# Kernel optimization log

Measured on AMD Instinct MI355X. Metric: run time of the kernel, lower is better.

Reference implementation:

```python
import jax, jax.numpy as jnp
import numpy as np

B_, L_, D_ = 4, 4096, 256
EXPAND = 2
DI_ = EXPAND * D_      # 512 inner channels
H_ = 8                 # heads
P_ = DI_ // H_         # 64 head dim
N_ = 16                # d_state
K_ = 3                 # depthwise conv kernel


def setup_inputs() -> dict:
    key = jax.random.key(0)
    ks = jax.random.split(key, 32)

    def n(i, shape, s=0.02):
        return jax.random.normal(ks[i], shape, jnp.float32) * s

    inp = {"inputs": jax.random.normal(ks[0], (B_, L_, D_), jnp.float32)}
    i = 1
    for pre in ("f_", "b_"):
        inp[pre + "in_proj_w"] = n(i, (2 * DI_, D_)); i += 1
        inp[pre + "in_proj_b"] = jnp.zeros((2 * DI_,), jnp.float32)
        inp[pre + "x_proj_w"] = n(i, (DI_ + 2 * H_ * N_, DI_)); i += 1
        inp[pre + "x_proj_b"] = jnp.zeros((DI_ + 2 * H_ * N_,), jnp.float32)
        inp[pre + "dt_bias"] = jnp.full((DI_,), -4.0, jnp.float32)  # softplus -> small dt
        inp[pre + "A_log"] = jnp.log(jnp.tile(jnp.arange(1, N_ + 1, dtype=jnp.float32), (DI_, 1)))
        inp[pre + "D_skip"] = jnp.ones((DI_,), jnp.float32)
        inp[pre + "out_proj_w"] = n(i, (D_, DI_)); i += 1
        inp[pre + "out_proj_b"] = jnp.zeros((D_,), jnp.float32)
    inp["norm_w"] = jnp.ones((D_,), jnp.float32)
    inp["norm_b"] = jnp.zeros((D_,), jnp.float32)
    inp["conv_w"] = n(20, (D_, 1, K_), 0.1)   # depthwise: (out_ch, in_ch/groups=1, k)
    inp["conv_b"] = jnp.zeros((D_,), jnp.float32)
    return inp


def _layernorm(x, w, b):
    m = x.mean(-1, keepdims=True)
    v = ((x - m) ** 2).mean(-1, keepdims=True)
    return (x - m) * jax.lax.rsqrt(v + 1e-5) * w + b


def _mh_ssm(x, in_w, in_b, xp_w, xp_b, dt_b, A_log, D_skip, out_w, out_b):
    # Multihead selective-scan SSM (Mamba-style). x: (B, L, D)
    Bsz, L, _ = x.shape
    xz = x @ in_w.T + in_b                      # (B, L, 2*DI)
    xi, z = jnp.split(xz, 2, axis=-1)
    xi = jax.nn.silu(xi)                        # (B, L, DI)
    proj = xi @ xp_w.T + xp_b                   # (B, L, DI + 2*H*N)
    dt = jax.nn.softplus(proj[..., :DI_] + dt_b)        # (B, L, DI)
    Bm = proj[..., DI_:DI_ + H_ * N_].reshape(Bsz, L, H_, N_)
    Cm = proj[..., DI_ + H_ * N_:].reshape(Bsz, L, H_, N_)
    A = -jnp.exp(A_log).reshape(H_, P_, N_)     # (H, P, N), negative
    x4 = xi.reshape(Bsz, L, H_, P_)
    dt4 = dt.reshape(Bsz, L, H_, P_)

    def step(h, t):
        xt, dtt, Bt, Ct = t                     # (B,H,P), (B,H,P), (B,H,N), (B,H,N)
        dA = jnp.exp(dtt[..., None] * A)        # (B,H,P,N)
        h = h * dA + dtt[..., None] * Bt[:, :, None, :] * xt[..., None]
        y = jnp.einsum('bhpn,bhn->bhp', h, Ct)
        return h, y

    xs = (x4.transpose(1, 0, 2, 3), dt4.transpose(1, 0, 2, 3),
          Bm.transpose(1, 0, 2, 3), Cm.transpose(1, 0, 2, 3))
    h0 = jnp.zeros((Bsz, H_, P_, N_), x.dtype)
    _, ys = jax.lax.scan(step, h0, xs)          # ys: (L,B,H,P)
    y = ys.transpose(1, 0, 2, 3).reshape(Bsz, L, DI_) + xi * D_skip
    y = y * jax.nn.silu(z)                      # gating
    return y @ out_w.T + out_b                  # (B, L, D)


def reference(inputs,
              f_in_proj_w, f_in_proj_b, f_x_proj_w, f_x_proj_b, f_dt_bias,
              f_A_log, f_D_skip, f_out_proj_w, f_out_proj_b,
              b_in_proj_w, b_in_proj_b, b_x_proj_w, b_x_proj_b, b_dt_bias,
              b_A_log, b_D_skip, b_out_proj_w, b_out_proj_b,
              norm_w, norm_b, conv_w, conv_b):
    # Cascaded bidirectional SSM: backward(flip(norm(forward(x)))) then flip back
    y1 = _mh_ssm(inputs, f_in_proj_w, f_in_proj_b, f_x_proj_w, f_x_proj_b,
                 f_dt_bias, f_A_log, f_D_skip, f_out_proj_w, f_out_proj_b)
    y1n = jnp.flip(_layernorm(y1, norm_w, norm_b), axis=1)
    y2 = _mh_ssm(y1n, b_in_proj_w, b_in_proj_b, b_x_proj_w, b_x_proj_b,
                 b_dt_bias, b_A_log, b_D_skip, b_out_proj_w, b_out_proj_b)
    out = jnp.flip(y2, axis=1)
    # locality branch: depthwise Conv1d (groups=C) + exact GELU
    xt = inputs.transpose(0, 2, 1)              # (B, C, L)
    c = jax.lax.conv_general_dilated(
        xt, conv_w, window_strides=(1,), padding=[(1, 1)],
        dimension_numbers=('NCH', 'OIH', 'NCH'), feature_group_count=D_)
    c = jax.nn.gelu(c + conv_b[None, :, None], approximate=False)
    return out + c.transpose(0, 2, 1)
```

## Files before the change

### kernel.cpp

```cpp
#include <hip/hip_runtime.h>
#include <hip/hip_bf16.h>
#include <cstdint>
#include <cstddef>

#define B_  4
#define L_  4096
#define D_  256
#define DI_ 512
#define H_  8
#define P_  64
#define N_  16
#define M_  (B_ * L_)
#define PROJ_ (DI_ + 2 * H_ * N_)

#define NC_ 128
#define CL_ (L_ / NC_)
#define NSEQ_ (B_ * H_ * P_ * N_)
#define LOG2E_ 1.4426950408889634f

typedef __bf16 bf16x8 __attribute__((ext_vector_type(8)));
typedef float f32x4 __attribute__((ext_vector_type(4)));

__device__ __forceinline__ void cp16_lds(const __hip_bfloat16* g, short* lds) {
    __builtin_amdgcn_global_load_lds(
        (const __attribute__((address_space(1))) void*)g,
        (__attribute__((address_space(3))) void*)lds, 16, 0, 0);
}

#define FS0 (M_ * D_)
#define FS1 (2 * DI_ * D_)
#define FS2 (PROJ_ * DI_)
#define FS3 (D_ * DI_)
#define FC1 (FS0 + FS1)
#define FC2 (FC1 + FS2)
#define FC3 (FC2 + FS3)
#define FC4 (FC3 + FS1)
#define FC5 (FC4 + FS2)
#define FC6 (FC5 + FS3)

__launch_bounds__(256)
__global__ void f2b_all(const float* __restrict__ i0, const float* __restrict__ i1,
                        const float* __restrict__ i2, const float* __restrict__ i3,
                        const float* __restrict__ i4, const float* __restrict__ i5,
                        const float* __restrict__ i6,
                        __hip_bfloat16* o0, __hip_bfloat16* o1, __hip_bfloat16* o2,
                        __hip_bfloat16* o3, __hip_bfloat16* o4, __hip_bfloat16* o5,
                        __hip_bfloat16* o6) {
    for (int idx = blockIdx.x * 256 + threadIdx.x; idx < FC6; idx += gridDim.x * 256) {
        const float* s; __hip_bfloat16* d; int off;
        if (idx < FS0)      { s = i0; d = o0; off = idx; }
        else if (idx < FC1) { s = i1; d = o1; off = idx - FS0; }
        else if (idx < FC2) { s = i2; d = o2; off = idx - FC1; }
        else if (idx < FC3) { s = i3; d = o3; off = idx - FC2; }
        else if (idx < FC4) { s = i4; d = o4; off = idx - FC3; }
        else if (idx < FC5) { s = i5; d = o5; off = idx - FC4; }
        else                { s = i6; d = o6; off = idx - FC5; }
        d[off] = __float2bfloat16(s[off]);
    }
}

template <int EPI>
__launch_bounds__(256)
__global__ void gemm_mfma(const __hip_bfloat16* __restrict__ A,
                          const __hip_bfloat16* __restrict__ W,
                          const float* __restrict__ bias, int Kv,
                          __hip_bfloat16* __restrict__ zb,
                          __hip_bfloat16* __restrict__ obf,
                          const float* __restrict__ aux) {
    __shared__ short As[128 * 64];
    __shared__ short Bs[128 * 64];
    const int tid = threadIdx.x;
    const int lane = tid & 63;
    const int wave = tid >> 6;
    const int bm = blockIdx.x * 128;
    const int bn = blockIdx.y * 128;
    const int wm = (wave >> 1) * 64;
    const int wn = (wave & 1) * 64;

    f32x4 acc[4][4];
#pragma unroll
    for (int i = 0; i < 4; ++i)
#pragma unroll
        for (int j = 0; j < 4; ++j) acc[i][j] = (f32x4)0.f;

    const int srow = lane >> 3;
    const int ssegx = ((lane & 7) ^ srow) * 8;
    const __hip_bfloat16* gA0 = A + (size_t)(bm + wave * 32 + srow) * Kv + ssegx;
    const __hip_bfloat16* gB0 = W + (size_t)(bn + wave * 32 + srow) * Kv + ssegx;
    short* lA0 = As + (wave * 32) * 64;
    short* lB0 = Bs + (wave * 32) * 64;

    const int fr = lane & 15;
    const int kq = lane >> 4;

    for (int k0 = 0; k0 < Kv; k0 += 64) {
#pragma unroll
        for (int rb = 0; rb < 4; ++rb) {
            cp16_lds(gA0 + (size_t)(rb * 8) * Kv + k0, lA0 + rb * 8 * 64);
            cp16_lds(gB0 + (size_t)(rb * 8) * Kv + k0, lB0 + rb * 8 * 64);
        }
        __syncthreads();
#pragma unroll
        for (int ks = 0; ks < 2; ++ks) {
            const int kgg = ks * 4 + kq;
            const int kslot = (kgg ^ (fr & 7)) * 8;
            bf16x8 af[4], bv[4];
#pragma unroll
            for (int i = 0; i < 4; ++i)
                af[i] = *reinterpret_cast<const bf16x8*>(
                    &As[(wm + i * 16 + fr) * 64 + kslot]);
#pragma unroll
            for (int j = 0; j < 4; ++j)
                bv[j] = *reinterpret_cast<const bf16x8*>(
                    &Bs[(wn + j * 16 + fr) * 64 + kslot]);
#pragma unroll
            for (int i = 0; i < 4; ++i)
#pragma unroll
                for (int j = 0; j < 4; ++j)
                    acc[i][j] = __builtin_amdgcn_mfma_f32_16x16x32_bf16(
                        af[i], bv[j], acc[i][j], 0, 0, 0);
        }
        __syncthreads();
    }

    const int n16 = lane & 15;
    const int r4 = (lane >> 4) * 4;
#pragma unroll
    for (int i = 0; i < 4; ++i) {
#pragma unroll
        for (int j = 0; j < 4; ++j) {
            const int cg = bn + wn + j * 16 + n16;
            const float bb = bias[cg];
#pragma unroll
            for (int v = 0; v < 4; ++v) {
                const int r = bm + wm + i * 16 + r4 + v;
                float val = acc[i][j][v] + bb;
                if (EPI == 1) {
                    if (cg < DI_) {
                        val = val / (1.f + __expf(-val));
                        obf[(size_t)r * DI_ + cg] = __float2bfloat16(val);
                    } else {
                        zb[(size_t)r * DI_ + cg - DI_] = __float2bfloat16(val);
                    }
                } else {
                    if (cg < DI_) {
                        const float x = val + aux[cg];
                        val = (x > 20.f) ? x : __logf(1.f + __expf(x));
                    }
                    obf[(size_t)r * PROJ_ + cg] = __float2bfloat16(val);
                }
            }
        }
    }
}

__launch_bounds__(256)
__global__ void gemm64_convout(const __hip_bfloat16* __restrict__ A,
                               const __hip_bfloat16* __restrict__ W,
                               const float* __restrict__ bias, int Kv,
                               float* __restrict__ out0,
                               const float* __restrict__ cw,
                               const float* __restrict__ cb,
                               const float* __restrict__ cinp) {
    __shared__ short As[64 * 64];
    __shared__ short Bs[64 * 64];
    const int tid = threadIdx.x;
    const int lane = tid & 63;
    const int wave = tid >> 6;
    const int bm = blockIdx.x * 64;
    const int bn = blockIdx.y * 64;
    const int wm = (wave >> 1) * 32;
    const int wn = (wave & 1) * 32;

    f32x4 acc[2][2];
#pragma unroll
    for (int i = 0; i < 2; ++i)
#pragma unroll
        for (int j = 0; j < 2; ++j) acc[i][j] = (f32x4)0.f;

    const int srow = lane >> 3;
    const int ssegx = ((lane & 7) ^ srow) * 8;
    const __hip_bfloat16* gA0 = A + (size_t)(bm + wave * 16 + srow) * Kv + ssegx;
    const __hip_bfloat16* gB0 = W + (size_t)(bn + wave * 16 + srow) * Kv + ssegx;
    short* lA0 = As + (wave * 16) * 64;
    short* lB0 = Bs + (wave * 16) * 64;

    const int fr = lane & 15;
    const int kq = lane >> 4;

    for (int k0 = 0; k0 < Kv; k0 += 64) {
#pragma unroll
        for (int rb = 0; rb < 2; ++rb) {
            cp16_lds(gA0 + (size_t)(rb * 8) * Kv + k0, lA0 + rb * 8 * 64);
            cp16_lds(gB0 + (size_t)(rb * 8) * Kv + k0, lB0 + rb * 8 * 64);
        }
        __syncthreads();
#pragma unroll
        for (int ks = 0; ks < 2; ++ks) {
            const int kgg = ks * 4 + kq;
            const int kslot = (kgg ^ (fr & 7)) * 8;
            bf16x8 af[2], bv[2];
#pragma unroll
            for (int i = 0; i < 2; ++i)
                af[i] = *reinterpret_cast<const bf16x8*>(
                    &As[(wm + i * 16 + fr) * 64 + kslot]);
#pragma unroll
            for (int j = 0; j < 2; ++j)
                bv[j] = *reinterpret_cast<const bf16x8*>(
                    &Bs[(wn + j * 16 + fr) * 64 + kslot]);
#pragma unroll
            for (int i = 0; i < 2; ++i)
#pragma unroll
                for (int j = 0; j < 2; ++j)
                    acc[i][j] = __builtin_amdgcn_mfma_f32_16x16x32_bf16(
                        af[i], bv[j], acc[i][j], 0, 0, 0);
        }
        __syncthreads();
    }

    const int n16 = lane & 15;
    const int r4 = (lane >> 4) * 4;
#pragma unroll
    for (int i = 0; i < 2; ++i) {
#pragma unroll
        for (int j = 0; j < 2; ++j) {
            const int cg = bn + wn + j * 16 + n16;
            const float bb = bias[cg];
#pragma unroll
            for (int v = 0; v < 4; ++v) {
                const int r = bm + wm + i * 16 + r4 + v;
                float val = acc[i][j][v] + bb;
                const int b = r >> 12;
                const int l = r & (L_ - 1);
                const int lo = L_ - 1 - l;
                const size_t base = ((size_t)(b << 12) + lo) * 256 + cg;
                float cv = fmaf(cinp[base], cw[cg * 3 + 1], cb[cg]);
                if (lo > 0) cv = fmaf(cinp[base - 256], cw[cg * 3 + 0], cv);
                if (lo + 1 < L_) cv = fmaf(cinp[base + 256], cw[cg * 3 + 2], cv);
                const float g = 0.5f * cv * (1.f + erff(cv * 0.70710678118654752f));
                out0[base] = val + g;
            }
        }
    }
}

__launch_bounds__(256)
__global__ void gemm_out_ln(const __hip_bfloat16* __restrict__ A,
                            const __hip_bfloat16* __restrict__ W,
                            const float* __restrict__ bias,
                            const float* __restrict__ lnw,
                            const float* __restrict__ lnb,
                            __hip_bfloat16* __restrict__ outb) {
    __shared__ short As[16 * 64];
    __shared__ short Ws[256 * 64];
    __shared__ float rs[2][4][16];
    const int tid = threadIdx.x;
    const int lane = tid & 63;
    const int wave = tid >> 6;
    const int bm = blockIdx.x * 16;
    const int Kv = DI_;

    f32x4 acc[4];
#pragma unroll
    for (int j = 0; j < 4; ++j) acc[j] = (f32x4)0.f;

    const int srow = lane >> 3;
    const int ssegx = ((lane & 7) ^ srow) * 8;
    const __hip_bfloat16* gA0 = A + (size_t)(bm + wave * 8 + srow) * Kv + ssegx;
    const __hip_bfloat16* gW0 = W + (size_t)(wave * 64 + srow) * Kv + ssegx;
    short* lA0 = As + (wave * 8) * 64;
    short* lW0 = Ws + (wave * 64) * 64;

    const int fr = lane & 15;
    const int kq = lane >> 4;

    for (int k0 = 0; k0 < Kv; k0 += 64) {
        if (wave < 2) cp16_lds(gA0 + k0, lA0);
#pragma unroll
        for (int rb = 0; rb < 8; ++rb)
            cp16_lds(gW0 + (size_t)(rb * 8) * Kv + k0, lW0 + rb * 8 * 64);
        __syncthreads();
#pragma unroll
        for (int ks = 0; ks < 2; ++ks) {
            const int kgg = ks * 4 + kq;
            const int kslot = (kgg ^ (fr & 7)) * 8;
            const bf16x8 af = *reinterpret_cast<const bf16x8*>(
                &As[fr * 64 + kslot]);
#pragma unroll
            for (int j = 0; j < 4; ++j) {
                const bf16x8 bv = *reinterpret_cast<const bf16x8*>(
                    &Ws[(wave * 64 + j * 16 + fr) * 64 + kslot]);
                acc[j] = __builtin_amdgcn_mfma_f32_16x16x32_bf16(
                    af, bv, acc[j], 0, 0, 0);
            }
        }
        __syncthreads();
    }

    const int n16 = lane & 15;
    const int r4 = (lane >> 4) * 4;
    float vals[4][4];
#pragma unroll
    for (int j = 0; j < 4; ++j) {
        const float bb = bias[wave * 64 + j * 16 + n16];
#pragma unroll
        for (int v = 0; v < 4; ++v) vals[j][v] = acc[j][v] + bb;
    }

#pragma unroll
    for (int v = 0; v < 4; ++v) {
        float s = 0.f, s2 = 0.f;
#pragma unroll
        for (int j = 0; j < 4; ++j) {
            const float t = vals[j][v];
            s += t; s2 = fmaf(t, t, s2);
        }
        s += __shfl_xor(s, 1); s2 += __shfl_xor(s2, 1);
        s += __shfl_xor(s, 2); s2 += __shfl_xor(s2, 2);
        s += __shfl_xor(s, 4); s2 += __shfl_xor(s2, 4);
        s += __shfl_xor(s, 8); s2 += __shfl_xor(s2, 8);
        if (n16 == 0) {
            rs[0][wave][r4 + v] = s;
            rs[1][wave][r4 + v] = s2;
        }
    }
    __syncthreads();

#pragma unroll
    for (int v = 0; v < 4; ++v) {
        const int row = r4 + v;
        const float ts = rs[0][0][row] + rs[0][1][row] + rs[0][2][row] + rs[0][3][row];
        const float ts2 = rs[1][0][row] + rs[1][1][row] + rs[1][2][row] + rs[1][3][row];
        const float mean = ts * (1.f / 256.f);
        const float var = ts2 * (1.f / 256.f) - mean * mean;
        const float inv = rsqrtf(var + 1e-5f);
        const int rg = bm + row;
        const int b = rg >> 12;
        const int l = rg & (L_ - 1);
        const size_t drow = (size_t)((b << 12) + (L_ - 1 - l)) * 256;
#pragma unroll
        for (int j = 0; j < 4; ++j) {
            const int cg = wave * 64 + j * 16 + n16;
            const float o = (vals[j][v] - mean) * inv * lnw[cg] + lnb[cg];
            outb[drow + cg] = __float2bfloat16(o);
        }
    }
}

__device__ __forceinline__ bool a_is_arith(const float* A2) {
    bool ok = true;
#pragma unroll
    for (int n = 1; n < N_; ++n)
        ok = ok && (fabsf(A2[n] - (float)(n + 1) * A2[0]) <= 1e-4f * fabsf(A2[n]));
    return ok;
}

__launch_bounds__(256)
__global__ void scan_chunk_state(const __hip_bfloat16* __restrict__ xi,
                                 const __hip_bfloat16* __restrict__ projb,
                                 const float* __restrict__ A_log,
                                 float* __restrict__ st_prod,
                                 float* __restrict__ st_hend) {
    __shared__ float bsh[4][CL_][16];
    const int bh = blockIdx.x;
    const int b = bh >> 3;
    const int h = bh & 7;
    const int lane = threadIdx.x & 63;
    const int wave = threadIdx.x >> 6;
    const int chunk = blockIdx.y * 4 + wave;
    const int t0 = chunk * CL_;
    const int c = h * P_ + lane;
    const int bOff = DI_ + h * N_;

    {
        const int stp = lane >> 1;
        const int half = (lane & 1) * 8;
        const __hip_bfloat16* src =
            projb + ((size_t)b * L_ + t0 + stp) * PROJ_ + bOff + half;
        const bf16x8 v = *reinterpret_cast<const bf16x8*>(src);
        float4* dst = reinterpret_cast<float4*>(&bsh[wave][stp][half]);
        dst[0] = make_float4((float)v[0], (float)v[1], (float)v[2], (float)v[3]);
        dst[1] = make_float4((float)v[4], (float)v[5], (float)v[6], (float)v[7]);
    }

    float A2[N_], hs[N_];
#pragma unroll
    for (int n = 0; n < N_; ++n) {
        A2[n] = -__expf(A_log[c * N_ + n]) * LOG2E_;
        hs[n] = 0.f;
    }
    const bool fast = a_is_arith(A2);

    const __hip_bfloat16* pDt = projb + ((size_t)b * L_ + t0) * PROJ_ + c;
    const __hip_bfloat16* px = xi + ((size_t)b * L_ + t0) * DI_ + c;
    float S = 0.f;

    if (fast) {
        float dtb[2][4], xb[2][4];
#pragma unroll
        for (int i = 0; i < 4; ++i) {
            dtb[0][i] = __bfloat162float(pDt[(size_t)i * PROJ_]);
            xb[0][i] = __bfloat162float(px[(size_t)i * DI_]);
        }
#pragma unroll
        for (int k = 0; k < CL_ / 4; ++k) {
            const int cur = k & 1, nxt = cur ^ 1;
            if (k + 1 < CL_ / 4) {
#pragma unroll
                for (int i = 0; i < 4; ++i) {
                    dtb[nxt][i] = __bfloat162float(pDt[(size_t)((k + 1) * 4 + i) * PROJ_]);
                    xb[nxt][i] = __bfloat162float(px[(size_t)((k + 1) * 4 + i) * DI_]);
                }
            }
#pragma unroll
            for (int i = 0; i < 4; ++i) {
                const int t = k * 4 + i;
                const float dt_v = dtb[cur][i];
                const float dtx = dt_v * xb[cur][i];
                const float e1 = exp2f(dt_v * A2[0]);
                S += dt_v;
                const f32x4* bp = reinterpret_cast<const f32x4*>(&bsh[wave][t][0]);
                float dA = e1;
#pragma unroll
                for (int q = 0; q < 4; ++q) {
                    const f32x4 Bq = bp[q];
#pragma unroll
                    for (int j = 0; j < 4; ++j) {
                        hs[q * 4 + j] = fmaf(hs[q * 4 + j], dA, dtx * Bq[j]);
                        dA *= e1;
                    }
                }
            }
        }
    } else {
#pragma unroll 4
        for (int t = 0; t < CL_; ++t) {
            const float dt_v = __bfloat162float(pDt[(size_t)t * PROJ_]);
            const float xv = __bfloat162float(px[(size_t)t * DI_]);
            const float dtx = dt_v * xv;
            S += dt_v;
#pragma unroll
            for (int n = 0; n < N_; ++n) {
                const float dA = exp2f(dt_v * A2[n]);
                hs[n] = fmaf(hs[n], dA, dtx * bsh[wave][t][n]);
            }
        }
    }

    const size_t s0 = (size_t)chunk * NSEQ_ + ((size_t)(bh * P_ + lane)) * N_;
#pragma unroll
    for (int n = 0; n < N_; n += 4) {
        *reinterpret_cast<float4*>(st_prod + s0 + n) =
            make_float4(exp2f(A2[n] * S), exp2f(A2[n + 1] * S),
                        exp2f(A2[n + 2] * S), exp2f(A2[n + 3] * S));
        *reinterpret_cast<float4*>(st_hend + s0 + n) =
            make_float4(hs[n], hs[n + 1], hs[n + 2], hs[n + 3]);
    }
}

__launch_bounds__(256)
__global__ void scan_combine(float* __restrict__ st_prod,
                             const float* __restrict__ st_hend) {
    const int s = blockIdx.x * 256 + threadIdx.x;
    float H = 0.f;
#pragma unroll 8
    for (int k = 0; k < NC_; ++k) {
        const size_t o = (size_t)k * NSEQ_ + s;
        const float Pv = st_prod[o];
        const float Ev = st_hend[o];
        st_prod[o] = H;
        H = fmaf(Pv, H, Ev);
    }
}

__launch_bounds__(256)
__global__ void scan_chunk_out(const __hip_bfloat16* __restrict__ xi,
                               const __hip_bfloat16* __restrict__ z,
                               const __hip_bfloat16* __restrict__ projb,
                               const float* __restrict__ A_log,
                               const float* __restrict__ D_skip,
                               const float* __restrict__ st_hin,
                               __hip_bfloat16* __restrict__ yg) {
    __shared__ float bc[4][CL_][32];
    const int bh = blockIdx.x;
    const int b = bh >> 3;
    const int h = bh & 7;
    const int lane = threadIdx.x & 63;
    const int wave = threadIdx.x >> 6;
    const int chunk = blockIdx.y * 4 + wave;
    const int t0 = chunk * CL_;
    const int c = h * P_ + lane;
    const int bOff = DI_ + h * N_;
    const int cOff = DI_ + H_ * N_ + h * N_;

    {
#pragma unroll
        for (int r = 0; r < 2; ++r) {
            const int g = r * 64 + lane;
            const int stp = g >> 2;
            const int q = g & 3;
            const int soff = (q < 2) ? (bOff + q * 8) : (cOff + (q - 2) * 8);
            const __hip_bfloat16* src =
                projb + ((size_t)b * L_ + t0 + stp) * PROJ_ + soff;
            const bf16x8 v = *reinterpret_cast<const bf16x8*>(src);
            float4* dst = reinterpret_cast<float4*>(&bc[wave][stp][q * 8]);
            dst[0] = make_float4((float)v[0], (float)v[1], (float)v[2], (float)v[3]);
            dst[1] = make_float4((float)v[4], (float)v[5], (float)v[6], (float)v[7]);
        }
    }

    float A2[N_], hs[N_];
    const size_t s0 = (size_t)chunk * NSEQ_ + ((size_t)(bh * P_ + lane)) * N_;
#pragma unroll
    for (int n = 0; n < N_; n += 4) {
        const float4 h4 = *reinterpret_cast<const float4*>(st_hin + s0 + n);
        hs[n] = h4.x; hs[n + 1] = h4.y; hs[n + 2] = h4.z; hs[n + 3] = h4.w;
    }
#pragma unroll
    for (int n = 0; n < N_; ++n)
        A2[n] = -__expf(A_log[c * N_ + n]) * LOG2E_;
    const bool fast = a_is_arith(A2);
    const float Dv = D_skip[c];

    const __hip_bfloat16* pDt = projb + ((size_t)b * L_ + t0) * PROJ_ + c;
    const __hip_bfloat16* px = xi + ((size_t)b * L_ + t0) * DI_ + c;
    const __hip_bfloat16* pz = z + ((size_t)b * L_ + t0) * DI_ + c;
    __hip_bfloat16* py = yg + ((size_t)b * L_ + t0) * DI_ + c;

    if (fast) {
        float dtb[2][4], xb[2][4], zb[2][4];
#pragma unroll
        for (int i = 0; i < 4; ++i) {
            dtb[0][i] = __bfloat162float(pDt[(size_t)i * PROJ_]);
            xb[0][i] = __bfloat162float(px[(size_t)i * DI_]);
            zb[0][i] = __bfloat162float(pz[(size_t)i * DI_]);
        }
#pragma unroll
        for (int k = 0; k < CL_ / 4; ++k) {
            const int cur = k & 1, nxt = cur ^ 1;
            if (k + 1 < CL_ / 4) {
#pragma unroll
                for (int i = 0; i < 4; ++i) {
                    const int t = (k + 1) * 4 + i;
                    dtb[nxt][i] = __bfloat162float(pDt[(size_t)t * PROJ_]);
                    xb[nxt][i] = __bfloat162float(px[(size_t)t * DI_]);
                    zb[nxt][i] = __bfloat162float(pz[(size_t)t * DI_]);
                }
            }
#pragma unroll
            for (int i = 0; i < 4; ++i) {
                const int t = k * 4 + i;
                const float dt_v = dtb[cur][i];
                const float xv = xb[cur][i];
                const float zv = zb[cur][i];
                const float dtx = dt_v * xv;
                const float e1 = exp2f(dt_v * A2[0]);
                const f32x4* bp = reinterpret_cast<const f32x4*>(&bc[wave][t][0]);
                float dA = e1;
                float y = 0.f;
#pragma unroll
                for (int q = 0; q < 4; ++q) {
                    const f32x4 Bq = bp[q];
                    const f32x4 Cq = bp[4 + q];
#pragma unroll
                    for (int j = 0; j < 4; ++j) {
                        hs[q * 4 + j] = fmaf(hs[q * 4 + j], dA, dtx * Bq[j]);
                        y = fmaf(hs[q * 4 + j], Cq[j], y);
                        dA *= e1;
                    }
                }
                const float g = zv / (1.f + __expf(-zv));
                py[(size_t)t * DI_] = __float2bfloat16((y + Dv * xv) * g);
            }
        }
    } else {
#pragma unroll 4
        for (int t = 0; t < CL_; ++t) {
            const float dt_v = __bfloat162float(pDt[(size_t)t * PROJ_]);
            const float xv = __bfloat162float(px[(size_t)t * DI_]);
            const float zv = __bfloat162float(pz[(size_t)t * DI_]);
            const float dtx = dt_v * xv;
            float y = 0.f;
#pragma unroll
            for (int n = 0; n < N_; ++n) {
                const float dA = exp2f(dt_v * A2[n]);
                hs[n] = fmaf(hs[n], dA, dtx * bc[wave][t][n]);
                y = fmaf(hs[n], bc[wave][t][16 + n], y);
            }
            const float g = zv / (1.f + __expf(-zv));
            py[(size_t)t * DI_] = __float2bfloat16((y + Dv * xv) * g);
        }
    }
}

extern "C" void kernel_launch(void* const* d_in, const int* in_sizes, int n_in,
                              void* d_out, int out_size, void* d_ws, size_t ws_size,
                              hipStream_t stream) {
    const float* inputs = (const float*)d_in[0];
    const float* f_in_w = (const float*)d_in[1];
    const float* f_in_b = (const float*)d_in[2];
    const float* f_xp_w = (const float*)d_in[3];
    const float* f_xp_b = (const float*)d_in[4];
    const float* f_dt_b = (const float*)d_in[5];
    const float* f_A = (const float*)d_in[6];
    const float* f_D = (const float*)d_in[7];
    const float* f_out_w = (const float*)d_in[8];
    const float* f_out_b = (const float*)d_in[9];
    const float* b_in_w = (const float*)d_in[10];
    const float* b_in_b = (const float*)d_in[11];
    const float* b_xp_w = (const float*)d_in[12];
    const float* b_xp_b = (const float*)d_in[13];
    const float* b_dt_b = (const float*)d_in[14];
    const float* b_A = (const float*)d_in[15];
    const float* b_D = (const float*)d_in[16];
    const float* b_out_w = (const float*)d_in[17];
    const float* b_out_b = (const float*)d_in[18];
    const float* norm_w = (const float*)d_in[19];
    const float* norm_b = (const float*)d_in[20];
    const float* conv_w = (const float*)d_in[21];
    const float* conv_b = (const float*)d_in[22];
    float* out = (float*)d_out;

    float* ws = (float*)d_ws;
    float* st_prod = ws;
    float* st_hend = st_prod + (size_t)NSEQ_ * NC_;
    float* zslot   = st_hend + (size_t)NSEQ_ * NC_;
    __hip_bfloat16* z_bf = (__hip_bfloat16*)zslot;
    float* pslot   = zslot + (size_t)M_ * DI_;
    __hip_bfloat16* proj_bf = (__hip_bfloat16*)pslot;
    float* y1      = pslot + (size_t)M_ * PROJ_;
    __hip_bfloat16* xi_bf = (__hip_bfloat16*)(y1 + (size_t)M_ * D_);
    __hip_bfloat16* yg_bf = xi_bf + (size_t)M_ * DI_;
    __hip_bfloat16* a_bf  = yg_bf + (size_t)M_ * DI_;
    __hip_bfloat16* wpool = a_bf + (size_t)M_ * D_;
    __hip_bfloat16* f_in_wb  = wpool;
    __hip_bfloat16* f_xp_wb  = f_in_wb + 2 * DI_ * D_;
    __hip_bfloat16* f_out_wb = f_xp_wb + PROJ_ * DI_;
    __hip_bfloat16* b_in_wb  = f_out_wb + D_ * DI_;
    __hip_bfloat16* b_xp_wb  = b_in_wb + 2 * DI_ * D_;
    __hip_bfloat16* b_out_wb = b_xp_wb + PROJ_ * DI_;

    const dim3 blk(256);
    const dim3 g_in(M_ / 128, (2 * DI_) / 128);
    const dim3 g_xp(M_ / 128, PROJ_ / 128);
    const dim3 g_out64(M_ / 64, D_ / 64);
    const dim3 g_oln(M_ / 16);
    const dim3 g_chunk(B_ * H_, NC_ / 4);
    const dim3 g_comb(NSEQ_ / 256);

    f2b_all<<<dim3(4096), blk, 0, stream>>>(inputs, f_in_w, f_xp_w, f_out_w,
                                            b_in_w, b_xp_w, b_out_w,
                                            a_bf, f_in_wb, f_xp_wb, f_out_wb,
                                            b_in_wb, b_xp_wb, b_out_wb);

    gemm_mfma<1><<<g_in, blk, 0, stream>>>(a_bf, f_in_wb, f_in_b, D_,
                                           z_bf, xi_bf, nullptr);
    gemm_mfma<2><<<g_xp, blk, 0, stream>>>(xi_bf, f_xp_wb, f_xp_b, DI_,
                                           nullptr, proj_bf, f_dt_b);
    scan_chunk_state<<<g_chunk, blk, 0, stream>>>(xi_bf, proj_bf, f_A,
                                                  st_prod, st_hend);
    scan_combine<<<g_comb, blk, 0, stream>>>(st_prod, st_hend);
    scan_chunk_out<<<g_chunk, blk, 0, stream>>>(xi_bf, z_bf, proj_bf, f_A, f_D,
                                                st_prod, yg_bf);
    gemm_out_ln<<<g_oln, blk, 0, stream>>>(yg_bf, f_out_wb, f_out_b,
                                           norm_w, norm_b, a_bf);

    gemm_mfma<1><<<g_in, blk, 0, stream>>>(a_bf, b_in_wb, b_in_b, D_,
                                           z_bf, xi_bf, nullptr);
    gemm_mfma<2><<<g_xp, blk, 0, stream>>>(xi_bf, b_xp_wb, b_xp_b, DI_,
                                           nullptr, proj_bf, b_dt_b);
    scan_chunk_state<<<g_chunk, blk, 0, stream>>>(xi_bf, proj_bf, b_A,
                                                  st_prod, st_hend);
    scan_combine<<<g_comb, blk, 0, stream>>>(st_prod, st_hend);
    scan_chunk_out<<<g_chunk, blk, 0, stream>>>(xi_bf, z_bf, proj_bf, b_A, b_D,
                                                st_prod, yg_bf);
    gemm64_convout<<<g_out64, blk, 0, stream>>>(yg_bf, b_out_wb, b_out_b, DI_,
                                                out, conv_w, conv_b, inputs);
}
```

Measured before the change: 395.9 us.

## Enlarge out-proj LN GEMM row tile and recompute chunk decay from dt sums

The fused out-projection plus LayerNorm GEMM now processes 64 rows per block instead of 16. This reuses each loaded weight tile across four times as many rows and cuts the grid size, at the cost of more accumulator registers. The chunk-state kernel stops writing the per-state decay products. It stores only the per-channel dt sum S, and the combine kernel recomputes exp2(A*S) on the fly. This removes a large float write and read of st_prod in exchange for extra exp work in the combine kernel.

```diff
diff --git a/kernel.cpp b/kernel.cpp
--- a/kernel.cpp
+++ b/kernel.cpp
@@ -251,31 +251,35 @@
                             const float* __restrict__ lnw,
                             const float* __restrict__ lnb,
                             __hip_bfloat16* __restrict__ outb) {
-    __shared__ short As[16 * 64];
+    __shared__ short As[64 * 64];
     __shared__ short Ws[256 * 64];
-    __shared__ float rs[2][4][16];
+    __shared__ float rs[2][4][64];
     const int tid = threadIdx.x;
     const int lane = tid & 63;
     const int wave = tid >> 6;
-    const int bm = blockIdx.x * 16;
+    const int bm = blockIdx.x * 64;
     const int Kv = DI_;
 
-    f32x4 acc[4];
-#pragma unroll
-    for (int j = 0; j < 4; ++j) acc[j] = (f32x4)0.f;
+    f32x4 acc[4][4];
+#pragma unroll
+    for (int i = 0; i < 4; ++i)
+#pragma unroll
+        for (int j = 0; j < 4; ++j) acc[i][j] = (f32x4)0.f;
 
     const int srow = lane >> 3;
     const int ssegx = ((lane & 7) ^ srow) * 8;
-    const __hip_bfloat16* gA0 = A + (size_t)(bm + wave * 8 + srow) * Kv + ssegx;
+    const __hip_bfloat16* gA0 = A + (size_t)(bm + wave * 16 + srow) * Kv + ssegx;
     const __hip_bfloat16* gW0 = W + (size_t)(wave * 64 + srow) * Kv + ssegx;
-    short* lA0 = As + (wave * 8) * 64;
+    short* lA0 = As + (wave * 16) * 64;
     short* lW0 = Ws + (wave * 64) * 64;
 
     const int fr = lane & 15;
     const int kq = lane >> 4;
 
     for (int k0 = 0; k0 < Kv; k0 += 64) {
-        if (wave < 2) cp16_lds(gA0 + k0, lA0);
+#pragma unroll
+        for (int rb = 0; rb < 2; ++rb)
+            cp16_lds(gA0 + (size_t)(rb * 8) * Kv + k0, lA0 + rb * 8 * 64);
 #pragma unroll
         for (int rb = 0; rb < 8; ++rb)
             cp16_lds(gW0 + (size_t)(rb * 8) * Kv + k0, lW0 + rb * 8 * 64);
@@ -284,65 +288,78 @@
         for (int ks = 0; ks < 2; ++ks) {
             const int kgg = ks * 4 + kq;
             const int kslot = (kgg ^ (fr & 7)) * 8;
-            const bf16x8 af = *reinterpret_cast<const bf16x8*>(
-                &As[fr * 64 + kslot]);
-#pragma unroll
-            for (int j = 0; j < 4; ++j) {
-                const bf16x8 bv = *reinterpret_cast<const bf16x8*>(
+            bf16x8 af[4], bv[4];
+#pragma unroll
+            for (int i = 0; i < 4; ++i)
+                af[i] = *reinterpret_cast<const bf16x8*>(
+                    &As[(i * 16 + fr) * 64 + kslot]);
+#pragma unroll
+            for (int j = 0; j < 4; ++j)
+                bv[j] = *reinterpret_cast<const bf16x8*>(
                     &Ws[(wave * 64 + j * 16 + fr) * 64 + kslot]);
-                acc[j] = __builtin_amdgcn_mfma_f32_16x16x32_bf16(
-                    af, bv, acc[j], 0, 0, 0);
-            }
+#pragma unroll
+            for (int i = 0; i < 4; ++i)
+#pragma unroll
+                for (int j = 0; j < 4; ++j)
+                    acc[i][j] = __builtin_amdgcn_mfma_f32_16x16x32_bf16(
+                        af[i], bv[j], acc[i][j], 0, 0, 0);
         }
         __syncthreads();
     }
 
     const int n16 = lane & 15;
     const int r4 = (lane >> 4) * 4;
-    float vals[4][4];
 #pragma unroll
     for (int j = 0; j < 4; ++j) {
         const float bb = bias[wave * 64 + j * 16 + n16];
 #pragma unroll
-        for (int v = 0; v < 4; ++v) vals[j][v] = acc[j][v] + bb;
-    }
-
-#pragma unroll
-    for (int v = 0; v < 4; ++v) {
-        float s = 0.f, s2 = 0.f;
-#pragma unroll
-        for (int j = 0; j < 4; ++j) {
-            const float t = vals[j][v];
-            s += t; s2 = fmaf(t, t, s2);
-        }
-        s += __shfl_xor(s, 1); s2 += __shfl_xor(s2, 1);
-        s += __shfl_xor(s, 2); s2 += __shfl_xor(s2, 2);
-        s += __shfl_xor(s, 4); s2 += __shfl_xor(s2, 4);
-        s += __shfl_xor(s, 8); s2 += __shfl_xor(s2, 8);
-        if (n16 == 0) {
-            rs[0][wave][r4 + v] = s;
-            rs[1][wave][r4 + v] = s2;
+        for (int i = 0; i < 4; ++i)
+#pragma unroll
+            for (int v = 0; v < 4; ++v) acc[i][j][v] += bb;
+    }
+
+#pragma unroll
+    for (int i = 0; i < 4; ++i) {
+#pragma unroll
+        for (int v = 0; v < 4; ++v) {
+            float s = 0.f, s2 = 0.f;
+#pragma unroll
+            for (int j = 0; j < 4; ++j) {
+                const float t = acc[i][j][v];
+                s += t; s2 = fmaf(t, t, s2);
+            }
+            s += __shfl_xor(s, 1); s2 += __shfl_xor(s2, 1);
+            s += __shfl_xor(s, 2); s2 += __shfl_xor(s2, 2);
+            s += __shfl_xor(s, 4); s2 += __shfl_xor(s2, 4);
+            s += __shfl_xor(s, 8); s2 += __shfl_xor(s2, 8);
+            if (n16 == 0) {
+                rs[0][wave][i * 16 + r4 + v] = s;
+                rs[1][wave][i * 16 + r4 + v] = s2;
+            }
         }
     }
     __syncthreads();
 
 #pragma unroll
-    for (int v = 0; v < 4; ++v) {
-        const int row = r4 + v;
-        const float ts = rs[0][0][row] + rs[0][1][row] + rs[0][2][row] + rs[0][3][row];
-        const float ts2 = rs[1][0][row] + rs[1][1][row] + rs[1][2][row] + rs[1][3][row];
-        const float mean = ts * (1.f / 256.f);
-        const float var = ts2 * (1.f / 256.f) - mean * mean;
-        const float inv = rsqrtf(var + 1e-5f);
-        const int rg = bm + row;
-        const int b = rg >> 12;
-        const int l = rg & (L_ - 1);
-        const size_t drow = (size_t)((b << 12) + (L_ - 1 - l)) * 256;
-#pragma unroll
-        for (int j = 0; j < 4; ++j) {
-            const int cg = wave * 64 + j * 16 + n16;
-            const float o = (vals[j][v] - mean) * inv * lnw[cg] + lnb[cg];
-            outb[drow + cg] = __float2bfloat16(o);
+    for (int i = 0; i < 4; ++i) {
+#pragma unroll
+        for (int v = 0; v < 4; ++v) {
+            const int row = i * 16 + r4 + v;
+            const float ts = rs[0][0][row] + rs[0][1][row] + rs[0][2][row] + rs[0][3][row];
+            const float ts2 = rs[1][0][row] + rs[1][1][row] + rs[1][2][row] + rs[1][3][row];
+            const float mean = ts * (1.f / 256.f);
+            const float var = ts2 * (1.f / 256.f) - mean * mean;
+            const float inv = rsqrtf(var + 1e-5f);
+            const int rg = bm + row;
+            const int b = rg >> 12;
+            const int l = rg & (L_ - 1);
+            const size_t drow = (size_t)((b << 12) + (L_ - 1 - l)) * 256;
+#pragma unroll
+            for (int j = 0; j < 4; ++j) {
+                const int cg = wave * 64 + j * 16 + n16;
+                const float o = (acc[i][j][v] - mean) * inv * lnw[cg] + lnb[cg];
+                outb[drow + cg] = __float2bfloat16(o);
+            }
         }
     }
 }
@@ -359,7 +376,7 @@
 __global__ void scan_chunk_state(const __hip_bfloat16* __restrict__ xi,
                                  const __hip_bfloat16* __restrict__ projb,
                                  const float* __restrict__ A_log,
-                                 float* __restrict__ st_prod,
+                                 float* __restrict__ sS,
                                  float* __restrict__ st_hend) {
     __shared__ float bsh[4][CL_][16];
     const int bh = blockIdx.x;
@@ -447,26 +464,30 @@
         }
     }
 
+    sS[(size_t)chunk * (B_ * DI_) + (size_t)(bh * P_ + lane)] = S;
     const size_t s0 = (size_t)chunk * NSEQ_ + ((size_t)(bh * P_ + lane)) * N_;
 #pragma unroll
     for (int n = 0; n < N_; n += 4) {
-        *reinterpret_cast<float4*>(st_prod + s0 + n) =
-            make_float4(exp2f(A2[n] * S), exp2f(A2[n + 1] * S),
-                        exp2f(A2[n + 2] * S), exp2f(A2[n + 3] * S));
         *reinterpret_cast<float4*>(st_hend + s0 + n) =
             make_float4(hs[n], hs[n + 1], hs[n + 2], hs[n + 3]);
     }
 }
 
-__launch_bounds__(256)
-__global__ void scan_combine(float* __restrict__ st_prod,
+__launch_bounds__(128)
+__global__ void scan_combine(const float* __restrict__ sS,
+                             const float* __restrict__ A_log,
+                             float* __restrict__ st_prod,
                              const float* __restrict__ st_hend) {
-    const int s = blockIdx.x * 256 + threadIdx.x;
+    const int s = blockIdx.x * 128 + threadIdx.x;
+    const int seqc = s >> 4;
+    const int n = s & 15;
+    const int cA = seqc & (DI_ - 1);
+    const float A2n = -__expf(A_log[cA * N_ + n]) * LOG2E_;
     float H = 0.f;
 #pragma unroll 8
     for (int k = 0; k < NC_; ++k) {
         const size_t o = (size_t)k * NSEQ_ + s;
-        const float Pv = st_prod[o];
+        const float Pv = exp2f(A2n * sS[(size_t)k * (B_ * DI_) + seqc]);
         const float Ev = st_hend[o];
         st_prod[o] = H;
         H = fmaf(Pv, H, Ev);
@@ -629,6 +650,7 @@
     float* pslot   = zslot + (size_t)M_ * DI_;
     __hip_bfloat16* proj_bf = (__hip_bfloat16*)pslot;
     float* y1      = pslot + (size_t)M_ * PROJ_;
+    float* sS      = y1;
     __hip_bfloat16* xi_bf = (__hip_bfloat16*)(y1 + (size_t)M_ * D_);
     __hip_bfloat16* yg_bf = xi_bf + (size_t)M_ * DI_;
     __hip_bfloat16* a_bf  = yg_bf + (size_t)M_ * DI_;
@@ -644,9 +666,10 @@
     const dim3 g_in(M_ / 128, (2 * DI_) / 128);
     const dim3 g_xp(M_ / 128, PROJ_ / 128);
     const dim3 g_out64(M_ / 64, D_ / 64);
-    const dim3 g_oln(M_ / 16);
+    const dim3 g_oln(M_ / 64);
     const dim3 g_chunk(B_ * H_, NC_ / 4);
-    const dim3 g_comb(NSEQ_ / 256);
+    const dim3 g_comb(NSEQ_ / 128);
+    const dim3 blk_comb(128);
 
     f2b_all<<<dim3(4096), blk, 0, stream>>>(inputs, f_in_w, f_xp_w, f_out_w,
                                             b_in_w, b_xp_w, b_out_w,
@@ -658,8 +681,8 @@
     gemm_mfma<2><<<g_xp, blk, 0, stream>>>(xi_bf, f_xp_wb, f_xp_b, DI_,
                                            nullptr, proj_bf, f_dt_b);
     scan_chunk_state<<<g_chunk, blk, 0, stream>>>(xi_bf, proj_bf, f_A,
-                                                  st_prod, st_hend);
-    scan_combine<<<g_comb, blk, 0, stream>>>(st_prod, st_hend);
+                                                  sS, st_hend);
+    scan_combine<<<g_comb, blk_comb, 0, stream>>>(sS, f_A, st_prod, st_hend);
     scan_chunk_out<<<g_chunk, blk, 0, stream>>>(xi_bf, z_bf, proj_bf, f_A, f_D,
                                                 st_prod, yg_bf);
     gemm_out_ln<<<g_oln, blk, 0, stream>>>(yg_bf, f_out_wb, f_out_b,
@@ -670,8 +693,8 @@
     gemm_mfma<2><<<g_xp, blk, 0, stream>>>(xi_bf, b_xp_wb, b_xp_b, DI_,
                                            nullptr, proj_bf, b_dt_b);
     scan_chunk_state<<<g_chunk, blk, 0, stream>>>(xi_bf, proj_bf, b_A,
-                                                  st_prod, st_hend);
-    scan_combine<<<g_comb, blk, 0, stream>>>(st_prod, st_hend);
+                                                  sS, st_hend);
+    scan_combine<<<g_comb, blk_comb, 0, stream>>>(sS, b_A, st_prod, st_hend);
     scan_chunk_out<<<g_chunk, blk, 0, stream>>>(xi_bf, z_bf, proj_bf, b_A, b_D,
                                                 st_prod, yg_bf);
     gemm64_convout<<<g_out64, blk, 0, stream>>>(yg_bf, b_out_wb, b_out_b, DI_,
```

Measured after the change: 384.3 us. 2.9% less time.
